# Optimization experiments

Hardware: AMD Instinct MI355X
Metric: run time of the kernel (lower is better)

The kernel has to match this reference:

```python
import jax, jax.numpy as jnp
import numpy as np

B, T, C = 4, 2048, 1024
NH = 16
HS = C // NH


def setup_inputs() -> dict:
    key = jax.random.key(0)
    k1, k2, k3, k4, k5 = jax.random.split(key, 5)
    scale = 1.0 / np.sqrt(C)
    return {
        "x": jax.random.normal(k1, (B, T, C), dtype=jnp.float32),
        "Wk": jax.random.normal(k2, (C, C), dtype=jnp.float32) * scale,
        "Wq": jax.random.normal(k3, (C, C), dtype=jnp.float32) * scale,
        "Wv": jax.random.normal(k4, (C, C), dtype=jnp.float32) * scale,
        "Wp": jax.random.normal(k5, (C, C), dtype=jnp.float32) * scale,
    }


def reference(x, Wk, Wq, Wv, Wp):
    b, t, c = x.shape
    # projections (nn.Linear with bias=False computes x @ W.T; weights here are
    # stored so that x @ W is equivalent -- same math, random init either way)
    k = (x @ Wk).reshape(b, t, NH, HS).transpose(0, 2, 1, 3)  # [B,H,T,hs]
    q = (x @ Wq).reshape(b, t, NH, HS).transpose(0, 2, 1, 3)
    v = (x @ Wv).reshape(b, t, NH, HS).transpose(0, 2, 1, 3)
    att = jnp.einsum("bhqd,bhkd->bhqk", q, k) / jnp.sqrt(jnp.float32(HS))
    causal = jnp.tril(jnp.ones((t, t), dtype=bool))
    att = jnp.where(causal[None, None, :, :], att, -jnp.inf)
    att = jax.nn.softmax(att, axis=-1)
    y = jnp.einsum("bhqk,bhkd->bhqd", att, v)  # [B,H,T,hs]
    y = y.transpose(0, 2, 1, 3).reshape(b, t, c)
    return y @ Wp
```

## Files before the change

kernel.cpp:

```cpp
#include <hip/hip_runtime.h>
#include <cstddef>
#include <cstdint>


namespace {

typedef unsigned short u16;
typedef unsigned int u32;
typedef __attribute__((ext_vector_type(8))) short s8v;
typedef __attribute__((ext_vector_type(4))) short s4v;
typedef __attribute__((ext_vector_type(4))) float f4v;

constexpr int Bn = 4, Tn = 2048, Cn = 1024;
constexpr int Mn = Bn * Tn;
constexpr int KVB = 128;
constexpr int NT128 = Tn / 128;
constexpr float QSCALE = 0.125f * 1.44269504f;

__device__ __forceinline__ u16 bfc(float f) {
  return __builtin_bit_cast(u16, (__bf16)f);
}

__device__ __forceinline__ float ex2(float x) {
#if __has_builtin(__builtin_amdgcn_exp2f)
  return __builtin_amdgcn_exp2f(x);
#else
  return exp2f(x);
#endif
}

__device__ __forceinline__ f4v mfma16(s8v a, s8v b, f4v c) {
  return __builtin_amdgcn_mfma_f32_16x16x32_bf16(a, b, c, 0, 0, 0);
}

__device__ __forceinline__ f4v mfma16k16(s4v a, s4v b, f4v c) {
#if __has_builtin(__builtin_amdgcn_mfma_f32_16x16x16bf16_1k)
  return __builtin_amdgcn_mfma_f32_16x16x16bf16_1k(a, b, c, 0, 0, 0);
#else
  f4v d = c;
  asm("v_mfma_f32_16x16x16_bf16 %0, %1, %2, %0" : "+v"(d) : "v"(a), "v"(b));
  return d;
#endif
}

typedef __attribute__((address_space(1))) const u32 gas_u32;
typedef __attribute__((address_space(3))) u32 las_u32;
__device__ __forceinline__ void gl_lds16(const void* g, void* l) {
  __builtin_amdgcn_global_load_lds((gas_u32*)g, (las_u32*)l, 16, 0, 0);
}

__global__ __launch_bounds__(256) void cvtx(const float* __restrict__ in,
                                            u16* __restrict__ out) {
  const size_t i = ((size_t)blockIdx.x * 256 + threadIdx.x) * 8;
  const float4 a = *(const float4*)(in + i);
  const float4 b = *(const float4*)(in + i + 4);
  alignas(16) u16 t[8] = {bfc(a.x), bfc(a.y), bfc(a.z), bfc(a.w),
                          bfc(b.x), bfc(b.y), bfc(b.z), bfc(b.w)};
  *(s8v*)(out + i) = *(const s8v*)t;
}

__global__ __launch_bounds__(256) void wtrans(
    const float* __restrict__ w0, const float* __restrict__ w1,
    const float* __restrict__ w2, const float* __restrict__ w3,
    u16* __restrict__ o0, u16* __restrict__ o1, u16* __restrict__ o2,
    u16* __restrict__ o3) {
  const float* W;
  u16* O;
  switch (blockIdx.z) {
    case 0: W = w0; O = o0; break;
    case 1: W = w1; O = o1; break;
    case 2: W = w2; O = o2; break;
    default: W = w3; O = o3; break;
  }
  __shared__ float Tsh[64][65];
  const int tid = threadIdx.x;
  const int n0 = blockIdx.x * 64, k0 = blockIdx.y * 64;
  {
    const int rk = tid >> 2, c0 = (tid & 3) * 16;
#pragma unroll
    for (int u = 0; u < 4; ++u) {
      const float4 v = *(const float4*)&W[(size_t)(k0 + rk) * Cn + n0 + c0 + u * 4];
      Tsh[rk][c0 + u * 4 + 0] = v.x;
      Tsh[rk][c0 + u * 4 + 1] = v.y;
      Tsh[rk][c0 + u * 4 + 2] = v.z;
      Tsh[rk][c0 + u * 4 + 3] = v.w;
    }
  }
  __syncthreads();
  {
    const int rn = tid >> 2, ck0 = (tid & 3) * 16;
    alignas(16) u16 t[16];
#pragma unroll
    for (int u = 0; u < 16; ++u) t[u] = bfc(Tsh[ck0 + u][rn]);
    *(s8v*)&O[(size_t)(n0 + rn) * Cn + k0 + ck0] = *(const s8v*)&t[0];
    *(s8v*)&O[(size_t)(n0 + rn) * Cn + k0 + ck0 + 8] = *(const s8v*)&t[8];
  }
}

template <int OUT_MODE>
__device__ __forceinline__ void gemm_body(const u16* __restrict__ A,
                                          const u16* __restrict__ Bt,
                                          void* __restrict__ Cout, int bm,
                                          int bn, u16* As, u16* Bs) {
  const int N = Cn, K = Cn;
  const int tid = threadIdx.x;
  const int l = tid & 63, w = tid >> 6;
  const int lr = l & 15, lh = l >> 4;
  const int lrow = tid >> 2;
  const int lkcol = (tid & 3) * 8;
  const u16* Ag = A + (size_t)(bm * 128 + lrow) * K + lkcol;
  const u16* Bg = Bt + (size_t)(bn * 128 + lrow) * K + lkcol;
  const int wm = (w >> 1) * 64, wn = (w & 1) * 64;
  f4v acc[4][4] = {};
  for (int k0 = 0; k0 < K; k0 += 32) {
    __syncthreads();
    gl_lds16(Ag + k0, &As[(size_t)tid * 8]);
    gl_lds16(Ag + (size_t)64 * K + k0, &As[2048 + (size_t)tid * 8]);
    gl_lds16(Bg + k0, &Bs[(size_t)tid * 8]);
    gl_lds16(Bg + (size_t)64 * K + k0, &Bs[2048 + (size_t)tid * 8]);
    __syncthreads();
    s8v af[4], bfr[4];
#pragma unroll
    for (int i = 0; i < 4; ++i)
      af[i] = *(const s8v*)&As[(wm + i * 16 + lr) * 32 + lh * 8];
#pragma unroll
    for (int j = 0; j < 4; ++j)
      bfr[j] = *(const s8v*)&Bs[(wn + j * 16 + lr) * 32 + lh * 8];
    __builtin_amdgcn_s_setprio(1);
#pragma unroll
    for (int i = 0; i < 4; ++i)
#pragma unroll
      for (int j = 0; j < 4; ++j)
        acc[i][j] = mfma16(af[i], bfr[j], acc[i][j]);
    __builtin_amdgcn_s_setprio(0);
  }
  if (OUT_MODE == 2) {
    float* Cf = (float*)Cout;
#pragma unroll
    for (int i = 0; i < 4; ++i) {
      const int row = bm * 128 + wm + i * 16 + lh * 4;
#pragma unroll
      for (int j = 0; j < 4; ++j) {
        const int col = bn * 128 + wn + j * 16 + lr;
#pragma unroll
        for (int r = 0; r < 4; ++r)
          Cf[(size_t)(row + r) * N + col] = acc[i][j][r];
      }
    }
  } else if (OUT_MODE == 0 || OUT_MODE == 3) {
    u16* Cb = (u16*)Cout;
    const float sc = (OUT_MODE == 3) ? QSCALE : 1.0f;
#pragma unroll
    for (int i = 0; i < 4; ++i) {
      const int row = bm * 128 + wm + i * 16 + lh * 4;
#pragma unroll
      for (int j = 0; j < 4; ++j) {
        const int col = bn * 128 + wn + j * 16 + lr;
#pragma unroll
        for (int r = 0; r < 4; ++r)
          Cb[(size_t)(row + r) * N + col] = bfc(acc[i][j][r] * sc);
      }
    }
  } else {
    u16* Vt = (u16*)Cout;
#pragma unroll
    for (int i = 0; i < 4; ++i) {
      const int row0 = bm * 128 + wm + i * 16 + lh * 4;
      const int bq = row0 >> 11, t0 = row0 & 2047;
#pragma unroll
      for (int j = 0; j < 4; ++j) {
        const int col = bn * 128 + wn + j * 16 + lr;
        const int hh = col >> 6, dd = col & 63;
        alignas(8) u16 t4[4];
#pragma unroll
        for (int r = 0; r < 4; ++r) t4[r] = bfc(acc[i][j][r]);
        *(s4v*)&Vt[((size_t)((bq * 16 + hh) * 64 + dd)) * Tn + t0] =
            *(const s4v*)t4;
      }
    }
  }
}

__global__ __launch_bounds__(256) void gemm_qkv(
    const u16* __restrict__ A, const u16* __restrict__ btq,
    const u16* __restrict__ btk, const u16* __restrict__ btv,
    u16* __restrict__ qb, u16* __restrict__ kb, u16* __restrict__ vt) {
  __shared__ __align__(16) u16 As[4096], Bs[4096];
  const int bid = blockIdx.x;
  const int wg = (bid & 7) * 192 + (bid >> 3);
  const int which = wg >> 9, inner = wg & 511;
  const int bm = inner & 63, bn = inner >> 6;
  if (which == 0)
    gemm_body<3>(A, btq, qb, bm, bn, As, Bs);
  else if (which == 1)
    gemm_body<0>(A, btk, kb, bm, bn, As, Bs);
  else
    gemm_body<1>(A, btv, vt, bm, bn, As, Bs);
}

template <int OUT_MODE>
__global__ __launch_bounds__(256) void gemm_bt(const u16* __restrict__ A,
                                               const u16* __restrict__ Bt,
                                               void* __restrict__ Cout) {
  __shared__ __align__(16) u16 As[4096], Bs[4096];
  const int bid = blockIdx.x;
  const int wg = (bid & 7) * 64 + (bid >> 3);
  const int bm = wg & 63, bn = wg >> 6;
  gemm_body<OUT_MODE>(A, Bt, Cout, bm, bn, As, Bs);
}

__device__ __forceinline__ void stage_kv(const u16* __restrict__ kgb,
                                         const u16* __restrict__ vtb,
                                         u16* __restrict__ Kb,
                                         u16* __restrict__ Vb, int k0,
                                         int tid) {
#pragma unroll
  for (int is = 0; is < 2; ++is) {
    const int slot = is * 512 + tid;
    const int row = slot >> 3, ch = slot & 7;
    gl_lds16(kgb + (size_t)(k0 + row) * Cn + ((ch ^ (row & 7)) * 8),
             &Kb[slot * 8]);
  }
#pragma unroll
  for (int is = 0; is < 2; ++is) {
    const int slot = is * 512 + tid;
    const int d = slot >> 4, ch = slot & 15;
    gl_lds16(vtb + (size_t)d * Tn + k0 + ((ch ^ (d & 7)) * 8), &Vb[slot * 8]);
  }
}

__device__ __forceinline__ void attn_step(const s8v* aq,
                                          const u16* __restrict__ Ks,
                                          const u16* __restrict__ Vs, int ln,
                                          int w, int lr, int lh, bool diag,
                                          int k0, int q0, float& m_i,
                                          float& l_i, f4v* o) {
  f4v s[8] = {};
  {
    const int sw = lr & 7;
    __builtin_amdgcn_s_setprio(1);
#pragma unroll
    for (int n = 0; n < 8; ++n) {
      const int rk = n * 16 + lr;
#pragma unroll
      for (int kd = 0; kd < 2; ++kd) {
        const s8v bk = *(const s8v*)&Ks[rk * 64 + (((kd * 4 + lh) ^ sw) * 8)];
        s[n] = mfma16(bk, aq[kd], s[n]);
      }
    }
    __builtin_amdgcn_s_setprio(0);
  }
  const int qg = q0 + w * 16 + lr;
  float rm = -1e30f;
  if (diag) {
#pragma unroll
    for (int n = 0; n < 8; ++n)
#pragma unroll
      for (int r = 0; r < 4; ++r) {
        float x = s[n][r];
        if (k0 + n * 16 + lh * 4 + r > qg) x = -1e30f;
        s[n][r] = x;
        rm = fmaxf(rm, x);
      }
  } else {
#pragma unroll
    for (int n = 0; n < 8; ++n)
      rm = fmaxf(rm, fmaxf(fmaxf(s[n][0], s[n][1]), fmaxf(s[n][2], s[n][3])));
  }
  if (!__all(rm <= m_i + 11.5f)) {
    float rr = fmaxf(rm, __shfl_xor(rm, 16));
    rr = fmaxf(rr, __shfl_xor(rr, 32));
    const float mnew = fmaxf(m_i, rr);
    const float al = ex2(m_i - mnew);
    m_i = mnew;
    l_i *= al;
#pragma unroll
    for (int r = 0; r < 4; ++r) {
      const float ar = __shfl(al, (ln & 48) | (lh * 4 + r));
#pragma unroll
      for (int n2 = 0; n2 < 4; ++n2) o[n2][r] *= ar;
    }
  }
  float rs = 0.f;
#pragma unroll
  for (int n = 0; n < 8; ++n) {
    const float p0 = ex2(s[n][0] - m_i);
    const float p1 = ex2(s[n][1] - m_i);
    const float p2 = ex2(s[n][2] - m_i);
    const float p3 = ex2(s[n][3] - m_i);
    rs += (p0 + p1) + (p2 + p3);
    const s4v pa = {(short)bfc(p0), (short)bfc(p1), (short)bfc(p2),
                    (short)bfc(p3)};
    __builtin_amdgcn_s_setprio(1);
#pragma unroll
    for (int n2 = 0; n2 < 4; ++n2) {
      const int d = n2 * 16 + lr;
      const int cl = (2 * n + (lh >> 1)) ^ (lr & 7);
      const s4v bv = *(const s4v*)&Vs[d * 128 + cl * 8 + (lh & 1) * 4];
      o[n2] = mfma16k16(pa, bv, o[n2]);
    }
    __builtin_amdgcn_s_setprio(0);
  }
  l_i += rs;
}

__global__ __launch_bounds__(512) void attn_big(const u16* __restrict__ qg,
                                                const u16* __restrict__ kg,
                                                const u16* __restrict__ vtg,
                                                u16* __restrict__ yg) {
  __shared__ __align__(16) u16 Ks0[KVB * 64], Ks1[KVB * 64];
  __shared__ __align__(16) u16 Vs0[64 * KVB], Vs1[64 * KVB];
  const int tid = threadIdx.x;
  const int ln = tid & 63, w = tid >> 6;
  const int lr = ln & 15, lh = ln >> 4;
  const int bid = blockIdx.x;
  const int wg = (bid & 7) * 64 + (bid >> 3);
  const int bh = wg >> 3, xp = wg & 7;
  const int b = bh >> 4, h = bh & 15;
  const int tL = xp, tH = NT128 - 1 - xp;
  const int q0L = tL * 128, q0H = tH * 128;
  const u16* kgb = kg + (size_t)(b * Tn) * Cn + h * 64;
  const u16* vtb = vtg + (size_t)(bh * 64) * Tn;
  s8v aqL[2], aqH[2];
  {
    const int row = w * 16 + lr;
#pragma unroll
    for (int kd = 0; kd < 2; ++kd) {
      aqL[kd] = *(const s8v*)&qg[(size_t)(b * Tn + q0L + row) * Cn + h * 64 +
                                 kd * 32 + lh * 8];
      aqH[kd] = *(const s8v*)&qg[(size_t)(b * Tn + q0H + row) * Cn + h * 64 +
                                 kd * 32 + lh * 8];
    }
  }
  float mL = -1e30f, lL = 0.f, mH = -1e30f, lH = 0.f;
  f4v oL[4] = {}, oH[4] = {};
  stage_kv(kgb, vtb, Ks0, Vs0, 0, tid);
  __syncthreads();
  for (int kt = 0; kt <= tH; ++kt) {
    const bool cur = kt & 1;
    const u16* Kb = cur ? Ks1 : Ks0;
    const u16* Vb = cur ? Vs1 : Vs0;
    if (kt < tH)
      stage_kv(kgb, vtb, cur ? Ks0 : Ks1, cur ? Vs0 : Vs1, (kt + 1) * KVB,
               tid);
    attn_step(aqH, Kb, Vb, ln, w, lr, lh, kt == tH, kt * KVB, q0H, mH, lH,
              oH);
    if (kt <= tL)
      attn_step(aqL, Kb, Vb, ln, w, lr, lh, kt == tL, kt * KVB, q0L, mL, lL,
                oL);
    __syncthreads();
  }
  {
    float ls = lH;
    ls += __shfl_xor(ls, 16);
    ls += __shfl_xor(ls, 32);
    const float linv = 1.0f / ls;
#pragma unroll
    for (int r = 0; r < 4; ++r) {
      const float iv = __shfl(linv, (ln & 48) | (lh * 4 + r));
      const int row = q0H + w * 16 + lh * 4 + r;
#pragma unroll
      for (int n2 = 0; n2 < 4; ++n2)
        yg[(size_t)(b * Tn + row) * Cn + h * 64 + n2 * 16 + lr] =
            bfc(oH[n2][r] * iv);
    }
  }
  {
    float ls = lL;
    ls += __shfl_xor(ls, 16);
    ls += __shfl_xor(ls, 32);
    const float linv = 1.0f / ls;
#pragma unroll
    for (int r = 0; r < 4; ++r) {
      const float iv = __shfl(linv, (ln & 48) | (lh * 4 + r));
      const int row = q0L + w * 16 + lh * 4 + r;
#pragma unroll
      for (int n2 = 0; n2 < 4; ++n2)
        yg[(size_t)(b * Tn + row) * Cn + h * 64 + n2 * 16 + lr] =
            bfc(oL[n2][r] * iv);
    }
  }
}

}

extern "C" void kernel_launch(void* const* d_in, const int* in_sizes, int n_in,
                              void* d_out, int out_size, void* d_ws,
                              size_t ws_size, hipStream_t stream) {
  (void)in_sizes; (void)n_in; (void)out_size; (void)ws_size;
  const float* x = (const float*)d_in[0];
  const float* Wk = (const float*)d_in[1];
  const float* Wq = (const float*)d_in[2];
  const float* Wv = (const float*)d_in[3];
  const float* Wp = (const float*)d_in[4];
  float* out = (float*)d_out;
  char* ws = (char*)d_ws;

  u16* xb = (u16*)(ws);
  u16* wqt = (u16*)(ws + 16777216);
  u16* wkt = (u16*)(ws + 18874368);
  u16* wvt = (u16*)(ws + 20971520);
  u16* wpt = (u16*)(ws + 23068672);
  u16* qb = (u16*)(ws + 25165824);
  u16* kb = (u16*)(ws + 41943040);
  u16* vt = (u16*)(ws + 58720256);
  u16* yb = (u16*)(ws + 75497472);

  cvtx<<<dim3(4096), dim3(256), 0, stream>>>(x, xb);
  wtrans<<<dim3(16, 16, 4), dim3(256), 0, stream>>>(Wq, Wk, Wv, Wp, wqt, wkt,
                                                    wvt, wpt);
  gemm_qkv<<<dim3(1536), dim3(256), 0, stream>>>(xb, wqt, wkt, wvt, qb, kb,
                                                 vt);
  attn_big<<<dim3(512), dim3(512), 0, stream>>>(qb, kb, vt, yb);
  gemm_bt<2><<<dim3(512), dim3(256), 0, stream>>>(yb, wpt, out);
}
```

Before: 196.9 us.

## Permute V-transpose layout so PV fragments load as 16-byte LDS reads

The QKV GEMM now writes the transposed V with a permutation of time indices inside each 128-token block. In the attention step, one 8-wide LDS read then supplies the operands for two consecutive k16 MFMAs instead of one 4-wide read per MFMA. The P fragments are buffered for all eight key groups before the PV MFMAs run. LDS addresses for K and V are precomputed once per thread and hoisted out of the step. This halves the number of V LDS instructions and trims address arithmetic. The cost is eight extra live s4v registers and a producer/consumer layout coupling that must stay consistent.

```diff
diff --git a/kernel.cpp b/kernel.cpp
--- a/kernel.cpp
+++ b/kernel.cpp
@@ -166,7 +166,12 @@
 #pragma unroll
     for (int i = 0; i < 4; ++i) {
       const int row0 = bm * 128 + wm + i * 16 + lh * 4;
-      const int bq = row0 >> 11, t0 = row0 & 2047;
+      const int bq = row0 >> 11;
+      const int t0g = row0 & 2047;
+      const int tau = t0g & 127;
+      const int taup = ((tau >> 5) << 5) | (((tau >> 2) & 3) << 3) |
+                       (((tau >> 4) & 1) << 2);
+      const int t0p = (t0g & ~127) | taup;
 #pragma unroll
       for (int j = 0; j < 4; ++j) {
         const int col = bn * 128 + wn + j * 16 + lr;
@@ -174,7 +179,7 @@
         alignas(8) u16 t4[4];
 #pragma unroll
         for (int r = 0; r < 4; ++r) t4[r] = bfc(acc[i][j][r]);
-        *(s4v*)&Vt[((size_t)((bq * 16 + hh) * 64 + dd)) * Tn + t0] =
+        *(s4v*)&Vt[((size_t)((bq * 16 + hh) * 64 + dd)) * Tn + t0p] =
             *(const s4v*)t4;
       }
     }
@@ -229,28 +234,22 @@
   }
 }
 
-__device__ __forceinline__ void attn_step(const s8v* aq,
+__device__ __forceinline__ void attn_step(const s8v (&aq)[2],
                                           const u16* __restrict__ Ks,
-                                          const u16* __restrict__ Vs, int ln,
-                                          int w, int lr, int lh, bool diag,
-                                          int k0, int q0, float& m_i,
-                                          float& l_i, f4v* o) {
+                                          const u16* __restrict__ Vs, int kb0,
+                                          int kb1, const int (&vch)[4], int ln,
+                                          int lh, bool diag, int k0, int qg,
+                                          float& m_i, float& l_i, f4v* o) {
   f4v s[8] = {};
-  {
-    const int sw = lr & 7;
-    __builtin_amdgcn_s_setprio(1);
-#pragma unroll
-    for (int n = 0; n < 8; ++n) {
-      const int rk = n * 16 + lr;
-#pragma unroll
-      for (int kd = 0; kd < 2; ++kd) {
-        const s8v bk = *(const s8v*)&Ks[rk * 64 + (((kd * 4 + lh) ^ sw) * 8)];
-        s[n] = mfma16(bk, aq[kd], s[n]);
-      }
-    }
-    __builtin_amdgcn_s_setprio(0);
-  }
-  const int qg = q0 + w * 16 + lr;
+  __builtin_amdgcn_s_setprio(1);
+#pragma unroll
+  for (int n = 0; n < 8; ++n) {
+    const s8v bk0 = *(const s8v*)&Ks[kb0 + n * 1024];
+    const s8v bk1 = *(const s8v*)&Ks[kb1 + n * 1024];
+    s[n] = mfma16(bk0, aq[0], s[n]);
+    s[n] = mfma16(bk1, aq[1], s[n]);
+  }
+  __builtin_amdgcn_s_setprio(0);
   float rm = -1e30f;
   if (diag) {
 #pragma unroll
@@ -281,6 +280,7 @@
       for (int n2 = 0; n2 < 4; ++n2) o[n2][r] *= ar;
     }
   }
+  s4v pa[8];
   float rs = 0.f;
 #pragma unroll
   for (int n = 0; n < 8; ++n) {
@@ -289,19 +289,23 @@
     const float p2 = ex2(s[n][2] - m_i);
     const float p3 = ex2(s[n][3] - m_i);
     rs += (p0 + p1) + (p2 + p3);
-    const s4v pa = {(short)bfc(p0), (short)bfc(p1), (short)bfc(p2),
-                    (short)bfc(p3)};
-    __builtin_amdgcn_s_setprio(1);
-#pragma unroll
-    for (int n2 = 0; n2 < 4; ++n2) {
-      const int d = n2 * 16 + lr;
-      const int cl = (2 * n + (lh >> 1)) ^ (lr & 7);
-      const s4v bv = *(const s4v*)&Vs[d * 128 + cl * 8 + (lh & 1) * 4];
-      o[n2] = mfma16k16(pa, bv, o[n2]);
-    }
-    __builtin_amdgcn_s_setprio(0);
+    pa[n] = (s4v){(short)bfc(p0), (short)bfc(p1), (short)bfc(p2),
+                  (short)bfc(p3)};
   }
   l_i += rs;
+  __builtin_amdgcn_s_setprio(1);
+#pragma unroll
+  for (int n2 = 0; n2 < 4; ++n2) {
+#pragma unroll
+    for (int p = 0; p < 4; ++p) {
+      const s8v vv = *(const s8v*)&Vs[vch[p] + n2 * 2048];
+      const s4v lo = {vv[0], vv[1], vv[2], vv[3]};
+      const s4v hi = {vv[4], vv[5], vv[6], vv[7]};
+      o[n2] = mfma16k16(pa[2 * p], lo, o[n2]);
+      o[n2] = mfma16k16(pa[2 * p + 1], hi, o[n2]);
+    }
+  }
+  __builtin_amdgcn_s_setprio(0);
 }
 
 __global__ __launch_bounds__(512) void attn_big(const u16* __restrict__ qg,
@@ -321,6 +325,12 @@
   const int q0L = tL * 128, q0H = tH * 128;
   const u16* kgb = kg + (size_t)(b * Tn) * Cn + h * 64;
   const u16* vtb = vtg + (size_t)(bh * 64) * Tn;
+  const int kb0 = lr * 64 + ((lh) ^ (lr & 7)) * 8;
+  const int kb1 = lr * 64 + ((4 + lh) ^ (lr & 7)) * 8;
+  int vch[4];
+#pragma unroll
+  for (int p = 0; p < 4; ++p)
+    vch[p] = lr * 128 + ((p * 4 + lh) ^ (lr & 7)) * 8;
   s8v aqL[2], aqH[2];
   {
     const int row = w * 16 + lr;
@@ -332,6 +342,8 @@
                                  kd * 32 + lh * 8];
     }
   }
+  const int qgH = q0H + w * 16 + lr;
+  const int qgL = q0L + w * 16 + lr;
   float mL = -1e30f, lL = 0.f, mH = -1e30f, lH = 0.f;
   f4v oL[4] = {}, oH[4] = {};
   stage_kv(kgb, vtb, Ks0, Vs0, 0, tid);
@@ -343,11 +355,11 @@
     if (kt < tH)
       stage_kv(kgb, vtb, cur ? Ks0 : Ks1, cur ? Vs0 : Vs1, (kt + 1) * KVB,
                tid);
-    attn_step(aqH, Kb, Vb, ln, w, lr, lh, kt == tH, kt * KVB, q0H, mH, lH,
-              oH);
+    attn_step(aqH, Kb, Vb, kb0, kb1, vch, ln, lh, kt == tH, kt * KVB, qgH, mH,
+              lH, oH);
     if (kt <= tL)
-      attn_step(aqL, Kb, Vb, ln, w, lr, lh, kt == tL, kt * KVB, q0L, mL, lL,
-                oL);
+      attn_step(aqL, Kb, Vb, kb0, kb1, vch, ln, lh, kt == tL, kt * KVB, qgL,
+                mL, lL, oL);
     __syncthreads();
   }
   {
```

Result: faster. 186.6 us (-5.3%).
